# Kernel tuning notes

Measured on AMD Instinct MI355X. Metric: run time of the kernel, lower is better.

The kernel has to match this reference:

```python
import jax, jax.numpy as jnp
import numpy as np

N_NODES = 50000
N_EDGES = 1_600_000
IN_DIM = 256
OUT_DIM = 128
NEG_SLOPE = 0.01  # F.leaky_relu default


def setup_inputs() -> dict:
    key = jax.random.key(0)
    k1, k2, k3, k4, k5 = jax.random.split(key, 5)
    x = jax.random.normal(k1, (N_NODES, IN_DIM), dtype=jnp.float32)
    # glorot_init: uniform in [-r, r], r = sqrt(6/(in+out))
    r = np.sqrt(6.0 / (IN_DIM + OUT_DIM)).astype(np.float32)
    weight = jax.random.uniform(k2, (IN_DIM, OUT_DIM), dtype=jnp.float32, minval=-r, maxval=r)
    adj_rows = jax.random.randint(k3, (N_EDGES,), 0, N_NODES, dtype=jnp.int64 if jax.config.jax_enable_x64 else jnp.int32)
    adj_cols = jax.random.randint(k4, (N_EDGES,), 0, N_NODES, dtype=jnp.int64 if jax.config.jax_enable_x64 else jnp.int32)
    adj_vals = jax.random.uniform(k5, (N_EDGES,), dtype=jnp.float32)
    return {"x": x, "weight": weight, "adj_vals": adj_vals,
            "adj_rows": adj_rows, "adj_cols": adj_cols}


def reference(x, weight, adj_vals, adj_rows, adj_cols):
    # h = X @ W : [N, OUT_DIM]
    h = x @ weight
    # sparse adj @ h via edge-list SpMM: out[r] += v * h[c]
    msgs = adj_vals[:, None] * h[adj_cols]            # [E, OUT_DIM]
    agg = jax.ops.segment_sum(msgs, adj_rows, num_segments=N_NODES)
    # leaky_relu epilogue
    return jnp.where(agg >= 0, agg, NEG_SLOPE * agg)
```

## Files before the change

kernel.cpp:

```cpp
#include <hip/hip_runtime.h>
#include <hip/hip_fp16.h>

#define N_NODES 50000
#define N_EDGES 1600000
#define IN_DIM 256
#define OUT_DIM 128
#define NEG_SLOPE 0.01f

#define SB_SH     10
#define SB_ROWS   1024
#define NSB       ((N_NODES + SB_ROWS - 1) / SB_ROWS)
#define SB_CAP    34816
#define PASSB_SPLIT 8
#define PB_ITERS  ((SB_CAP / PASSB_SPLIT + 511) / 512)

#define BIN_SH    5
#define BIN_ROWS  32
#define NBIN      ((N_NODES + BIN_ROWS - 1) / BIN_ROWS)
#define NBIN_PAD  (NSB * (SB_ROWS / BIN_ROWS))
#define CAPB      1280
#define OVF_CAP   65536

#define SCAT_BLOCKS 256
#define CONVW_BLOCKS 8
#define EPB_S (N_EDGES / SCAT_BLOCKS)
#define SCAT_ITERS ((EPB_S + 511) / 512)

typedef _Float16 f16x8 __attribute__((ext_vector_type(8)));
typedef float    f32x4 __attribute__((ext_vector_type(4)));
typedef float    f32x8 __attribute__((ext_vector_type(8)));

__device__ __forceinline__ float lrelu(float v) {
    return v >= 0.f ? v : NEG_SLOPE * v;
}

#define BM 128
#define GEMM_BLOCKS ((N_NODES + BM - 1) / BM)

#define CVT16(lo, hi) do { \
    lo[0]=(_Float16)xr[0].x; lo[1]=(_Float16)xr[0].y; lo[2]=(_Float16)xr[0].z; lo[3]=(_Float16)xr[0].w; \
    lo[4]=(_Float16)xr[1].x; lo[5]=(_Float16)xr[1].y; lo[6]=(_Float16)xr[1].z; lo[7]=(_Float16)xr[1].w; \
    hi[0]=(_Float16)xr[2].x; hi[1]=(_Float16)xr[2].y; hi[2]=(_Float16)xr[2].z; hi[3]=(_Float16)xr[2].w; \
    hi[4]=(_Float16)xr[3].x; hi[5]=(_Float16)xr[3].y; hi[6]=(_Float16)xr[3].z; hi[7]=(_Float16)xr[3].w; \
} while (0)

__global__ __launch_bounds__(256, 2) void gemm_xw_mfma(const float* __restrict__ x,
                                                       const __half* __restrict__ wtl,
                                                       __half* __restrict__ h) {
    __shared__ f16x8 wt8[32 * 128];
    __shared__ f16x8 xs8[2][4][BM];

    const int t    = threadIdx.x;
    const int lane = t & 63;
    const int wv   = t >> 6;
    const int row0 = blockIdx.x * BM;

    {
        const int4* src = (const int4*)wtl;
        int4* dst = (int4*)wt8;
#pragma unroll
        for (int i = 0; i < 16; ++i) dst[i * 256 + t] = src[i * 256 + t];
    }

    const int srow = t >> 1;
    const int skh  = t & 1;
    const int grow = row0 + srow;
    const bool rv  = grow < N_NODES;
    const float* xp = x + (size_t)(rv ? grow : 0) * IN_DIM + skh * 16;

    float4 xr[4];
#pragma unroll
    for (int i = 0; i < 4; ++i)
        xr[i] = rv ? ((const float4*)xp)[i] : make_float4(0.f, 0.f, 0.f, 0.f);
    {
        f16x8 lo, hi;
        CVT16(lo, hi);
        xs8[0][skh * 2 + 0][srow] = lo;
        xs8[0][skh * 2 + 1][srow] = hi;
    }
    __syncthreads();

    f32x4 acc[2][8];
#pragma unroll
    for (int mf = 0; mf < 2; ++mf)
#pragma unroll
        for (int nf = 0; nf < 8; ++nf) acc[mf][nf] = (f32x4){0.f, 0.f, 0.f, 0.f};

    const int kg  = lane >> 4;
    const int l15 = lane & 15;
    const int mb  = (wv << 5) + l15;

#pragma unroll
    for (int ks = 0; ks < 8; ++ks) {
        const int cur = ks & 1;
        if (ks < 7) {
#pragma unroll
            for (int i = 0; i < 4; ++i)
                xr[i] = rv ? ((const float4*)(xp + (ks + 1) * 32))[i]
                           : make_float4(0.f, 0.f, 0.f, 0.f);
        }
        const f16x8 b0 = xs8[cur][kg][mb];
        const f16x8 b1 = xs8[cur][kg][mb + 16];
#pragma unroll
        for (int nf = 0; nf < 8; ++nf) {
            const f16x8 a = wt8[(((ks << 2) | kg) << 7) + (nf << 4) + l15];
            acc[0][nf] = __builtin_amdgcn_mfma_f32_16x16x32_f16(a, b0, acc[0][nf], 0, 0, 0);
            acc[1][nf] = __builtin_amdgcn_mfma_f32_16x16x32_f16(a, b1, acc[1][nf], 0, 0, 0);
        }
        if (ks < 7) {
            f16x8 lo, hi;
            CVT16(lo, hi);
            xs8[cur ^ 1][skh * 2 + 0][srow] = lo;
            xs8[cur ^ 1][skh * 2 + 1][srow] = hi;
            __syncthreads();
        }
    }

    const int rg = lane >> 4;
#pragma unroll
    for (int mf = 0; mf < 2; ++mf) {
        const int m = row0 + (wv << 5) + (mf << 4) + l15;
        if (m < N_NODES) {
            __half* hp = h + (size_t)m * OUT_DIM + (rg << 2);
#pragma unroll
            for (int nf = 0; nf < 8; ++nf) {
                union { ushort4 u; __half f[4]; } o;
                o.f[0] = __float2half(acc[mf][nf][0]);
                o.f[1] = __float2half(acc[mf][nf][1]);
                o.f[2] = __float2half(acc[mf][nf][2]);
                o.f[3] = __float2half(acc[mf][nf][3]);
                *(ushort4*)(hp + (nf << 4)) = o.u;
            }
        }
    }
}

__global__ __launch_bounds__(512) void scatter_coarse(const int* __restrict__ rows,
                                                      const int* __restrict__ cols,
                                                      const float* __restrict__ vals,
                                                      int* __restrict__ sbcur,
                                                      int* __restrict__ ovfcnt,
                                                      int2* __restrict__ cbuf,
                                                      int2* __restrict__ ovfbuf,
                                                      const float* __restrict__ w,
                                                      __half* __restrict__ wtl) {
    if (blockIdx.x >= SCAT_BLOCKS) {
        const int e0 = ((blockIdx.x - SCAT_BLOCKS) * 512 + threadIdx.x) * 8;
        const int k  = e0 >> 7;
        const int n0 = e0 & 127;
        const float4 a = *(const float4*)(w + e0);
        const float4 b = *(const float4*)(w + e0 + 4);
        __half* dst = wtl + ((size_t)((k >> 3) * 128 + n0)) * 8 + (k & 7);
        dst[0]  = __float2half(a.x);
        dst[8]  = __float2half(a.y);
        dst[16] = __float2half(a.z);
        dst[24] = __float2half(a.w);
        dst[32] = __float2half(b.x);
        dst[40] = __float2half(b.y);
        dst[48] = __float2half(b.z);
        dst[56] = __float2half(b.w);
        return;
    }

    __shared__ int lcur[NSB];
    const int t = threadIdx.x;
    const int ebase = blockIdx.x * EPB_S;

    if (t < NSB) lcur[t] = 0;
    __syncthreads();

    int myr[SCAT_ITERS];
#pragma unroll
    for (int k = 0; k < SCAT_ITERS; ++k) {
        const int i = k * 512 + t;
        myr[k] = -1;
        if (i < EPB_S) {
            const int r = rows[ebase + i];
            myr[k] = r;
            atomicAdd(&lcur[r >> SB_SH], 1);
        }
    }
    __syncthreads();

    if (t < NSB) {
        const int c = lcur[t];
        lcur[t] = (c > 0) ? atomicAdd(&sbcur[t], c) : 0;
    }
    __syncthreads();

#pragma unroll
    for (int k = 0; k < SCAT_ITERS; ++k) {
        const int i = k * 512 + t;
        if (i < EPB_S) {
            const int e = ebase + i;
            const int r = myr[k];
            const int sb = r >> SB_SH;
            const int off = atomicAdd(&lcur[sb], 1);
            const int key = (int)(((unsigned)r << 16) | (unsigned)cols[e]);
            const int vb  = __float_as_int(vals[e]);
            if (off < SB_CAP) {
                cbuf[(size_t)sb * SB_CAP + off] = make_int2(key, vb);
            } else {
                const int p = atomicAdd(ovfcnt, 1);
                if (p < OVF_CAP) ovfbuf[p] = make_int2(key, vb);
            }
        }
    }
}

__global__ __launch_bounds__(512) void scatter_fine(const int* __restrict__ sbcur,
                                                    int* __restrict__ fcur,
                                                    int* __restrict__ ovfcnt,
                                                    const int2* __restrict__ cbuf,
                                                    int2* __restrict__ ebuf,
                                                    int2* __restrict__ ovfbuf) {
    __shared__ int lcur[SB_ROWS / BIN_ROWS];
    const int t    = threadIdx.x;
    const int sb   = blockIdx.x / PASSB_SPLIT;
    const int part = blockIdx.x % PASSB_SPLIT;

    const int cnt_sb = min(sbcur[sb], SB_CAP);
    const int chunk  = (cnt_sb + PASSB_SPLIT - 1) / PASSB_SPLIT;
    const int i0 = part * chunk;
    const int i1 = min(i0 + chunk, cnt_sb);

    if (t < 32) lcur[t] = 0;
    __syncthreads();

    int2 rc[PB_ITERS];
#pragma unroll
    for (int k = 0; k < PB_ITERS; ++k) {
        const int i = i0 + k * 512 + t;
        if (i < i1) {
            rc[k] = cbuf[(size_t)sb * SB_CAP + i];
            const unsigned urow = ((unsigned)rc[k].x) >> 16;
            atomicAdd(&lcur[(urow >> BIN_SH) & 31], 1);
        }
    }
    __syncthreads();

    if (t < 32) {
        const int c = lcur[t];
        lcur[t] = (c > 0) ? atomicAdd(&fcur[(sb << 5) + t], c) : 0;
    }
    __syncthreads();

#pragma unroll
    for (int k = 0; k < PB_ITERS; ++k) {
        const int i = i0 + k * 512 + t;
        if (i < i1) {
            const unsigned urow = ((unsigned)rc[k].x) >> 16;
            const int f   = (int)(urow >> BIN_SH);
            const int off = atomicAdd(&lcur[(urow >> BIN_SH) & 31], 1);
            const int key = (rc[k].x & 0xFFFF) | (int)((urow & (BIN_ROWS - 1)) << 16);
            if (off < CAPB) {
                ebuf[(size_t)f * CAPB + off] = make_int2(key, rc[k].y);
            } else {
                const int p = atomicAdd(ovfcnt, 1);
                if (p < OVF_CAP) ovfbuf[p] = rc[k];
            }
        }
    }
}

#define NCLS 256

#define STAGE(IT, HV, VV) do {                                                  \
    _Pragma("unroll")                                                           \
    for (int q = 0; q < 4; ++q) {                                               \
        const int idx = beg[q] + ((IT) << 2) + grp;                             \
        const bool vld = idx < end[q];                                          \
        const int2 r = srec[vld ? idx : 0];                                     \
        VV[q] = vld ? __int_as_float(r.y) : 0.f;                                \
        HV[q] = *(const f16x8*)(h + (size_t)(r.x & 0xFFFF) * OUT_DIM + (gl << 3)); \
    }                                                                           \
} while (0)

__global__ __launch_bounds__(512, 4) void sort_gather(const int* __restrict__ fcur,
                                                      const int* __restrict__ ovfcnt,
                                                      const int2* __restrict__ ebuf,
                                                      const int2* __restrict__ ovfbuf,
                                                      const __half* __restrict__ h,
                                                      float* __restrict__ out) {
    __shared__ int2 urec[CAPB];
    __shared__ int2 srec[CAPB];
    __shared__ int  hist[NCLS];
    __shared__ int  pfx[NCLS];
    __shared__ int  rowoff_l[BIN_ROWS + 1];
    __shared__ int  wsum[4];

    const int t    = threadIdx.x;
    const int bin  = blockIdx.x;
    const int wv   = t >> 6;
    const int lane = t & 63;

    const int cnt_all = fcur[bin];
    const int cnt     = cnt_all < CAPB ? cnt_all : CAPB;
    const size_t base = (size_t)bin * CAPB;

    if (t < NCLS) hist[t] = 0;
    __syncthreads();

    for (int i = t; i < cnt; i += 512) {
        const int2 r = ebuf[base + i];
        urec[i] = r;
        atomicAdd(&hist[(((r.x >> 16) & 31) << 3) | ((r.x & 0xFFFF) >> 13)], 1);
    }
    __syncthreads();

    {
        const int v = (t < NCLS) ? hist[t] : 0;
        int s = v;
#pragma unroll
        for (int off = 1; off < 64; off <<= 1) {
            const int u = __shfl_up(s, off);
            if (lane >= off) s += u;
        }
        if (t < NCLS && lane == 63) wsum[wv] = s;
        __syncthreads();
        if (t == 0) {
            int a = 0;
#pragma unroll
            for (int i = 0; i < 4; ++i) { const int c = wsum[i]; wsum[i] = a; a += c; }
        }
        __syncthreads();
        if (t < NCLS) {
            const int incl = s + wsum[wv];
            pfx[t]  = incl;
            hist[t] = incl - v;
        }
    }
    __syncthreads();
    if (t < BIN_ROWS) rowoff_l[t] = t ? pfx[(t << 3) - 1] : 0;
    if (t == BIN_ROWS) rowoff_l[BIN_ROWS] = cnt;
    __syncthreads();

    for (int i = t; i < cnt; i += 512) {
        const int2 r = urec[i];
        const int cls = (((r.x >> 16) & 31) << 3) | ((r.x & 0xFFFF) >> 13);
        const int pos = atomicAdd(&hist[cls], 1);
        srec[pos] = r;
    }
    __syncthreads();

    const int grp = lane >> 4;
    const int gl  = lane & 15;
    const int r0  = wv << 2;

    int beg[4], end[4];
#pragma unroll
    for (int q = 0; q < 4; ++q) { beg[q] = rowoff_l[r0 + q]; end[q] = rowoff_l[r0 + q + 1]; }
    int nmax = 0;
#pragma unroll
    for (int q = 0; q < 4; ++q) nmax = max(nmax, end[q] - beg[q]);
    const int iters = (nmax + 3) >> 2;

    f32x8 acc[4];
#pragma unroll
    for (int q = 0; q < 4; ++q) acc[q] = (f32x8){0.f,0.f,0.f,0.f,0.f,0.f,0.f,0.f};

    f16x8 hc[4], hn[4];
    float vc[4], vn[4];
    if (iters > 0) STAGE(0, hc, vc);
    for (int it = 0; it < iters; ++it) {
        if (it + 1 < iters) STAGE(it + 1, hn, vn);
#pragma unroll
        for (int q = 0; q < 4; ++q)
#pragma unroll
            for (int j = 0; j < 8; ++j) acc[q][j] += vc[q] * (float)hc[q][j];
#pragma unroll
        for (int q = 0; q < 4; ++q) { hc[q] = hn[q]; vc[q] = vn[q]; }
    }

    int novf = *ovfcnt;
    if (novf > OVF_CAP) novf = OVF_CAP;
    for (int e = 0; e < novf; ++e) {
        const int2 rec = ovfbuf[e];
        const unsigned urow = ((unsigned)rec.x) >> 16;
        if ((int)(urow >> BIN_SH) == bin && grp == 0) {
            const int lr = (int)(urow & (BIN_ROWS - 1)) - r0;
            if (lr >= 0 && lr < 4) {
                const float v = __int_as_float(rec.y);
                const f16x8 hv = *(const f16x8*)(h + (size_t)(rec.x & 0xFFFF) * OUT_DIM + (gl << 3));
#pragma unroll
                for (int q = 0; q < 4; ++q)
                    if (q == lr)
#pragma unroll
                        for (int j = 0; j < 8; ++j) acc[q][j] += v * (float)hv[j];
            }
        }
    }

#pragma unroll
    for (int q = 0; q < 4; ++q)
#pragma unroll
        for (int j = 0; j < 8; ++j) {
            float x = acc[q][j];
            x += __shfl_xor(x, 16);
            x += __shfl_xor(x, 32);
            acc[q][j] = x;
        }

    float res[8];
#pragma unroll
    for (int j = 0; j < 8; ++j) {
        float x = acc[0][j];
        x = (grp == 1) ? acc[1][j] : x;
        x = (grp == 2) ? acc[2][j] : x;
        x = (grp == 3) ? acc[3][j] : x;
        res[j] = lrelu(x);
    }
    const int grow = (bin << BIN_SH) + r0 + grp;
    if (grow < N_NODES) {
        float* op = out + (size_t)grow * OUT_DIM + (gl << 3);
        *(float4*)op       = make_float4(res[0], res[1], res[2], res[3]);
        *(float4*)(op + 4) = make_float4(res[4], res[5], res[6], res[7]);
    }
}

extern "C" void kernel_launch(void* const* d_in, const int* in_sizes, int n_in,
                              void* d_out, int out_size, void* d_ws, size_t ws_size,
                              hipStream_t stream) {
    const float* x    = (const float*)d_in[0];
    const float* w    = (const float*)d_in[1];
    const float* vals = (const float*)d_in[2];
    const int*   rows = (const int*)d_in[3];
    const int*   cols = (const int*)d_in[4];
    float* out = (float*)d_out;

    char* ws = (char*)d_ws;
    size_t off = 0;
    auto alloc = [&](size_t bytes) {
        void* p = ws + off;
        off = (off + bytes + 255) & ~(size_t)255;
        return p;
    };
    int2*  cbuf    = (int2*) alloc((size_t)NSB * SB_CAP * sizeof(int2));
    __half* h      = (__half*)cbuf;
    int2*  ebuf    = (int2*) alloc((size_t)NBIN * CAPB * sizeof(int2));
    int2*  ovfbuf  = (int2*) alloc((size_t)OVF_CAP * sizeof(int2));
    __half* wtl    = (__half*)alloc((size_t)IN_DIM * OUT_DIM * sizeof(__half));
    int*   meta    = (int*)  alloc((size_t)(NSB + NBIN_PAD + 1) * sizeof(int));
    int*   sbcur   = meta;
    int*   fcur    = meta + NSB;
    int*   ovfcnt  = meta + NSB + NBIN_PAD;

    hipMemsetAsync(meta, 0, (size_t)(NSB + NBIN_PAD + 1) * sizeof(int), stream);

    scatter_coarse<<<SCAT_BLOCKS + CONVW_BLOCKS, 512, 0, stream>>>(rows, cols, vals,
                                                                   sbcur, ovfcnt, cbuf, ovfbuf, w, wtl);
    scatter_fine<<<NSB * PASSB_SPLIT, 512, 0, stream>>>(sbcur, fcur, ovfcnt, cbuf, ebuf, ovfbuf);
    gemm_xw_mfma<<<GEMM_BLOCKS, 256, 0, stream>>>(x, wtl, h);
    sort_gather<<<NBIN, 512, 0, stream>>>(fcur, ovfcnt, ebuf, ovfbuf, h, out);
}
```

Measured before the change: 205.4 us.

## Replace global atomic bucket cursors with per-block fixed segments in scatter passes

The two-pass edge bucketing no longer uses global atomic cursors. Each scatter block now writes into its own fixed-size segment per super-bucket and records a count. The fine pass writes per-partition segments per bin, and sort_gather locates records through a prefix over the partition counts instead of a contiguous bin buffer. This removes the histogram pre-pass, the global atomics and most of the memset, and drops the urec shared buffer. The costs are more scattered reads of segmented memory, a larger workspace, and overflow spills whenever a segment exceeds its 208-entry capacity.

```diff
diff --git a/kernel.cpp b/kernel.cpp
--- a/kernel.cpp
+++ b/kernel.cpp
@@ -10,15 +10,14 @@
 #define SB_SH     10
 #define SB_ROWS   1024
 #define NSB       ((N_NODES + SB_ROWS - 1) / SB_ROWS)
-#define SB_CAP    34816
-#define PASSB_SPLIT 8
-#define PB_ITERS  ((SB_CAP / PASSB_SPLIT + 511) / 512)
+#define SEG       208
 
 #define BIN_SH    5
 #define BIN_ROWS  32
 #define NBIN      ((N_NODES + BIN_ROWS - 1) / BIN_ROWS)
-#define NBIN_PAD  (NSB * (SB_ROWS / BIN_ROWS))
-#define CAPB      1280
+#define NBIN_PAD  (NSB * 32)
+#define NPART     8
+#define CAPB_TOT  (NPART * SEG)
 #define OVF_CAP   65536
 
 #define SCAT_BLOCKS 256
@@ -138,7 +137,7 @@
 __global__ __launch_bounds__(512) void scatter_coarse(const int* __restrict__ rows,
                                                       const int* __restrict__ cols,
                                                       const float* __restrict__ vals,
-                                                      int* __restrict__ sbcur,
+                                                      int* __restrict__ ccnt,
                                                       int* __restrict__ ovfcnt,
                                                       int2* __restrict__ cbuf,
                                                       int2* __restrict__ ovfbuf,
@@ -164,28 +163,10 @@
 
     __shared__ int lcur[NSB];
     const int t = threadIdx.x;
-    const int ebase = blockIdx.x * EPB_S;
+    const int blk = blockIdx.x;
+    const int ebase = blk * EPB_S;
 
     if (t < NSB) lcur[t] = 0;
-    __syncthreads();
-
-    int myr[SCAT_ITERS];
-#pragma unroll
-    for (int k = 0; k < SCAT_ITERS; ++k) {
-        const int i = k * 512 + t;
-        myr[k] = -1;
-        if (i < EPB_S) {
-            const int r = rows[ebase + i];
-            myr[k] = r;
-            atomicAdd(&lcur[r >> SB_SH], 1);
-        }
-    }
-    __syncthreads();
-
-    if (t < NSB) {
-        const int c = lcur[t];
-        lcur[t] = (c > 0) ? atomicAdd(&sbcur[t], c) : 0;
-    }
     __syncthreads();
 
 #pragma unroll
@@ -193,74 +174,65 @@
         const int i = k * 512 + t;
         if (i < EPB_S) {
             const int e = ebase + i;
-            const int r = myr[k];
+            const int r = rows[e];
             const int sb = r >> SB_SH;
             const int off = atomicAdd(&lcur[sb], 1);
             const int key = (int)(((unsigned)r << 16) | (unsigned)cols[e]);
             const int vb  = __float_as_int(vals[e]);
-            if (off < SB_CAP) {
-                cbuf[(size_t)sb * SB_CAP + off] = make_int2(key, vb);
+            if (off < SEG) {
+                cbuf[((size_t)sb * SCAT_BLOCKS + blk) * SEG + off] = make_int2(key, vb);
             } else {
                 const int p = atomicAdd(ovfcnt, 1);
                 if (p < OVF_CAP) ovfbuf[p] = make_int2(key, vb);
             }
         }
     }
-}
-
-__global__ __launch_bounds__(512) void scatter_fine(const int* __restrict__ sbcur,
-                                                    int* __restrict__ fcur,
+    __syncthreads();
+
+    if (t < NSB) ccnt[t * SCAT_BLOCKS + blk] = min(lcur[t], SEG);
+}
+
+__global__ __launch_bounds__(512) void scatter_fine(const int* __restrict__ ccnt,
+                                                    int* __restrict__ fcnt,
                                                     int* __restrict__ ovfcnt,
                                                     const int2* __restrict__ cbuf,
                                                     int2* __restrict__ ebuf,
                                                     int2* __restrict__ ovfbuf) {
-    __shared__ int lcur[SB_ROWS / BIN_ROWS];
+    __shared__ int lcur[32];
+    __shared__ int scnt[32];
     const int t    = threadIdx.x;
-    const int sb   = blockIdx.x / PASSB_SPLIT;
-    const int part = blockIdx.x % PASSB_SPLIT;
-
-    const int cnt_sb = min(sbcur[sb], SB_CAP);
-    const int chunk  = (cnt_sb + PASSB_SPLIT - 1) / PASSB_SPLIT;
-    const int i0 = part * chunk;
-    const int i1 = min(i0 + chunk, cnt_sb);
-
-    if (t < 32) lcur[t] = 0;
-    __syncthreads();
-
-    int2 rc[PB_ITERS];
-#pragma unroll
-    for (int k = 0; k < PB_ITERS; ++k) {
-        const int i = i0 + k * 512 + t;
-        if (i < i1) {
-            rc[k] = cbuf[(size_t)sb * SB_CAP + i];
-            const unsigned urow = ((unsigned)rc[k].x) >> 16;
-            atomicAdd(&lcur[(urow >> BIN_SH) & 31], 1);
-        }
-    }
-    __syncthreads();
+    const int sb   = blockIdx.x / NPART;
+    const int p    = blockIdx.x % NPART;
+    const int wv   = t >> 6;
+    const int lane = t & 63;
 
     if (t < 32) {
-        const int c = lcur[t];
-        lcur[t] = (c > 0) ? atomicAdd(&fcur[(sb << 5) + t], c) : 0;
-    }
-    __syncthreads();
-
-#pragma unroll
-    for (int k = 0; k < PB_ITERS; ++k) {
-        const int i = i0 + k * 512 + t;
-        if (i < i1) {
-            const unsigned urow = ((unsigned)rc[k].x) >> 16;
-            const int f   = (int)(urow >> BIN_SH);
-            const int off = atomicAdd(&lcur[(urow >> BIN_SH) & 31], 1);
-            const int key = (rc[k].x & 0xFFFF) | (int)((urow & (BIN_ROWS - 1)) << 16);
-            if (off < CAPB) {
-                ebuf[(size_t)f * CAPB + off] = make_int2(key, rc[k].y);
+        lcur[t] = 0;
+        scnt[t] = ccnt[sb * SCAT_BLOCKS + p * 32 + t];
+    }
+    __syncthreads();
+
+    for (int j = 0; j < 4; ++j) {
+        const int seg = (wv << 2) + j;
+        const int cnt = scnt[seg];
+        const size_t sbase = ((size_t)sb * SCAT_BLOCKS + p * 32 + seg) * SEG;
+        for (int i = lane; i < cnt; i += 64) {
+            const int2 rc = cbuf[sbase + i];
+            const unsigned urow = ((unsigned)rc.x) >> 16;
+            const int fb = (int)((urow >> BIN_SH) & 31);
+            const int off = atomicAdd(&lcur[fb], 1);
+            const int key = (rc.x & 0xFFFF) | (int)((urow & (BIN_ROWS - 1)) << 16);
+            if (off < SEG) {
+                ebuf[(((size_t)sb * 32 + fb) * NPART + p) * SEG + off] = make_int2(key, rc.y);
             } else {
-                const int p = atomicAdd(ovfcnt, 1);
-                if (p < OVF_CAP) ovfbuf[p] = rc[k];
+                const int q = atomicAdd(ovfcnt, 1);
+                if (q < OVF_CAP) ovfbuf[q] = rc;
             }
         }
     }
+    __syncthreads();
+
+    if (t < 32) fcnt[((sb * 32 + t) * NPART) + p] = min(lcur[t], SEG);
 }
 
 #define NCLS 256
@@ -276,35 +248,45 @@
     }                                                                           \
 } while (0)
 
-__global__ __launch_bounds__(512, 4) void sort_gather(const int* __restrict__ fcur,
+__global__ __launch_bounds__(512, 4) void sort_gather(const int* __restrict__ fcnt,
                                                       const int* __restrict__ ovfcnt,
                                                       const int2* __restrict__ ebuf,
                                                       const int2* __restrict__ ovfbuf,
                                                       const __half* __restrict__ h,
                                                       float* __restrict__ out) {
-    __shared__ int2 urec[CAPB];
-    __shared__ int2 srec[CAPB];
+    __shared__ int2 srec[CAPB_TOT];
     __shared__ int  hist[NCLS];
     __shared__ int  pfx[NCLS];
     __shared__ int  rowoff_l[BIN_ROWS + 1];
     __shared__ int  wsum[4];
+    __shared__ int  poff[NPART + 1];
 
     const int t    = threadIdx.x;
     const int bin  = blockIdx.x;
     const int wv   = t >> 6;
     const int lane = t & 63;
 
-    const int cnt_all = fcur[bin];
-    const int cnt     = cnt_all < CAPB ? cnt_all : CAPB;
-    const size_t base = (size_t)bin * CAPB;
-
     if (t < NCLS) hist[t] = 0;
-    __syncthreads();
-
-    for (int i = t; i < cnt; i += 512) {
-        const int2 r = ebuf[base + i];
-        urec[i] = r;
-        atomicAdd(&hist[(((r.x >> 16) & 31) << 3) | ((r.x & 0xFFFF) >> 13)], 1);
+    if (t == 0) {
+        int a = 0;
+        poff[0] = 0;
+#pragma unroll
+        for (int p = 0; p < NPART; ++p) { a += fcnt[bin * NPART + p]; poff[p + 1] = a; }
+    }
+    __syncthreads();
+    const int cnt = poff[NPART];
+
+#define LOCATE(F, PP, II) do {                                                  \
+        PP = 0;                                                                 \
+        _Pragma("unroll")                                                       \
+        for (int j = 1; j < NPART; ++j) PP += ((F) >= poff[j]);                 \
+        II = (F) - poff[PP];                                                    \
+    } while (0)
+
+    for (int f = t; f < cnt; f += 512) {
+        int p, i; LOCATE(f, p, i);
+        const int k = ebuf[((size_t)bin * NPART + p) * SEG + i].x;
+        atomicAdd(&hist[(((k >> 16) & 31) << 3) | ((k & 0xFFFF) >> 13)], 1);
     }
     __syncthreads();
 
@@ -335,8 +317,9 @@
     if (t == BIN_ROWS) rowoff_l[BIN_ROWS] = cnt;
     __syncthreads();
 
-    for (int i = t; i < cnt; i += 512) {
-        const int2 r = urec[i];
+    for (int f = t; f < cnt; f += 512) {
+        int p, i; LOCATE(f, p, i);
+        const int2 r = ebuf[((size_t)bin * NPART + p) * SEG + i];
         const int cls = (((r.x >> 16) & 31) << 3) | ((r.x & 0xFFFF) >> 13);
         const int pos = atomicAdd(&hist[cls], 1);
         srec[pos] = r;
@@ -435,21 +418,20 @@
         off = (off + bytes + 255) & ~(size_t)255;
         return p;
     };
-    int2*  cbuf    = (int2*) alloc((size_t)NSB * SB_CAP * sizeof(int2));
+    int2*  cbuf    = (int2*) alloc((size_t)NSB * SCAT_BLOCKS * SEG * sizeof(int2));
     __half* h      = (__half*)cbuf;
-    int2*  ebuf    = (int2*) alloc((size_t)NBIN * CAPB * sizeof(int2));
+    int2*  ebuf    = (int2*) alloc((size_t)NBIN_PAD * NPART * SEG * sizeof(int2));
     int2*  ovfbuf  = (int2*) alloc((size_t)OVF_CAP * sizeof(int2));
     __half* wtl    = (__half*)alloc((size_t)IN_DIM * OUT_DIM * sizeof(__half));
-    int*   meta    = (int*)  alloc((size_t)(NSB + NBIN_PAD + 1) * sizeof(int));
-    int*   sbcur   = meta;
-    int*   fcur    = meta + NSB;
-    int*   ovfcnt  = meta + NSB + NBIN_PAD;
-
-    hipMemsetAsync(meta, 0, (size_t)(NSB + NBIN_PAD + 1) * sizeof(int), stream);
+    int*   ccnt    = (int*)  alloc((size_t)NSB * SCAT_BLOCKS * sizeof(int));
+    int*   fcnt    = (int*)  alloc((size_t)NBIN_PAD * NPART * sizeof(int));
+    int*   ovfcnt  = (int*)  alloc(sizeof(int));
+
+    hipMemsetAsync(ovfcnt, 0, sizeof(int), stream);
 
     scatter_coarse<<<SCAT_BLOCKS + CONVW_BLOCKS, 512, 0, stream>>>(rows, cols, vals,
-                                                                   sbcur, ovfcnt, cbuf, ovfbuf, w, wtl);
-    scatter_fine<<<NSB * PASSB_SPLIT, 512, 0, stream>>>(sbcur, fcur, ovfcnt, cbuf, ebuf, ovfbuf);
+                                                                   ccnt, ovfcnt, cbuf, ovfbuf, w, wtl);
+    scatter_fine<<<NSB * NPART, 512, 0, stream>>>(ccnt, fcnt, ovfcnt, cbuf, ebuf, ovfbuf);
     gemm_xw_mfma<<<GEMM_BLOCKS, 256, 0, stream>>>(x, wtl, h);
-    sort_gather<<<NBIN, 512, 0, stream>>>(fcur, ovfcnt, ebuf, ovfbuf, h, out);
-}
+    sort_gather<<<NBIN, 512, 0, stream>>>(fcnt, ovfcnt, ebuf, ovfbuf, h, out);
+}
```

Measured after the change: 198.2 us. 3.5% less time.
